# Optimization experiments

Hardware: AMD Instinct MI355X
Metric: run time of the kernel (lower is better)

## Reference

```python
import jax, jax.numpy as jnp
import numpy as np

B, L, IN, H, E = 64, 255, 32, 256, 128
PAD = (L - 1) // 2
DN = ('NCH', 'OIH', 'NCH')


def setup_inputs() -> dict:
    ks = jax.random.split(jax.random.key(0), 10)
    r = lambda k, shp, s=0.05: jax.random.normal(k, shp, dtype=jnp.float32) * s
    return {
        's': jax.random.normal(ks[0], (B, L, IN), dtype=jnp.float32),
        'conv1_w': r(ks[1], (H, IN, L)),
        'conv1_b': r(ks[2], (H,)),
        'bn_gamma': jnp.ones((H,), jnp.float32),
        'bn_beta': jnp.zeros((H,), jnp.float32),
        'conv2_w': r(ks[3], (E, H, L)),
        'conv2_b': r(ks[4], (E,)),
        'pw1': r(ks[5], (E, H, L)),   # stacked Linear(L, H) weights, one per channel
        'pb1': r(ks[6], (E, H)),
        'pw2': r(ks[7], (E, 2, H)),   # stacked Linear(H, 2) weights
        'pb2': r(ks[8], (E, 2)),
    }


def reference(s, conv1_w, conv1_b, bn_gamma, bn_beta, conv2_w, conv2_b, pw1, pb1, pw2, pb2):
    x = jnp.transpose(s, (0, 2, 1))  # (B, IN, T)
    h = jax.lax.conv_general_dilated(x, conv1_w, (1,), [(PAD, PAD)], dimension_numbers=DN)
    h = jax.nn.relu(h + conv1_b[None, :, None])
    # BatchNorm1d in training mode: biased batch stats over (N, T)
    mean = h.mean(axis=(0, 2), keepdims=True)
    var = ((h - mean) ** 2).mean(axis=(0, 2), keepdims=True)
    h = (h - mean) * jax.lax.rsqrt(var + 1e-5) * bn_gamma[None, :, None] + bn_beta[None, :, None]
    z = jax.lax.conv_general_dilated(h, conv2_w, (1,), [(PAD, PAD)], dimension_numbers=DN)
    z = jnp.transpose(z + conv2_b[None, :, None], (0, 2, 1))  # (B, T, E)

    rf = jnp.fft.rfft(z, axis=1)                 # (B, F, E), F = L//2 + 1 == E
    power = jnp.abs(rf)[:, :, 1:] ** 2           # faithful channel-axis slice -> (B, F, E-1)
    freq_bins = jnp.fft.rfftfreq(L)[1:]          # (F-1,) == (E-1,)
    frequency = jnp.sum(freq_bins * power, axis=1) / jnp.sum(power, axis=1)  # (B, E-1)
    amplitude = 2.0 * jnp.sqrt(jnp.sum(power, axis=1)) / L                    # (B, E-1)
    offset = rf.real[:, :, 0] / L                                              # (B, E)

    # batched per-channel 2-layer MLP (replaces Python loop over embedding_dim)
    hmid = jax.nn.relu(jnp.einsum('btc,cht->bch', z, pw1) + pb1[None])  # (B, E, H)
    ang = jnp.einsum('bch,coh->bco', hmid, pw2) + pb2[None]             # (B, E, 2)
    phase = jnp.arctan2(ang[:, :, 1], ang[:, :, 0])                     # (B, E)
    return (amplitude, phase, frequency, offset)
```

## Files before the change

### kernel.cpp

```cpp
#include <hip/hip_runtime.h>
#include <math.h>

#define TB   64
#define TT   255
#define TIN  32
#define NH   256
#define NE   128
#define NK   255
#define NPAD 127

#define NF    384
#define NBINS 193
#define NFC   386
#define HCH   64

typedef __attribute__((ext_vector_type(8))) short short8;
typedef __attribute__((ext_vector_type(4))) float float4v;

#define WSB_WP1  0u
#define WSB_Z    0u
#define WSB_W2S  8388608u
#define WSB_HSP  21037056u
#define WSB_ZSP  27361280u
#define WSB_BD   40009728u
#define WSB_BW   40404992u
#define WSB_BI   40800256u
#define WSB_H    41811968u
#define WSB_HMID 41811968u
#define WSB_BN   58589184u

#define O_AMP   0u
#define O_PHASE 8128u
#define O_FREQ  16320u
#define O_OFF   24448u

static __device__ __forceinline__ unsigned short f2bf(float f) {
  unsigned int u = __float_as_uint(f);
  unsigned int r = (u + 0x7FFFu + ((u >> 16) & 1u)) >> 16;
  return (unsigned short)r;
}
static __device__ __forceinline__ float bf2f(unsigned short s) {
  return __uint_as_float(((unsigned int)s) << 16);
}
static __device__ __forceinline__ short8 as_s8(uint4 v) {
  union { uint4 u; short8 s; } c; c.u = v; return c.s;
}

static __device__ __forceinline__ void stage8(unsigned int* __restrict__ U, int r,
                                              int p0, const float* __restrict__ v) {
  const int sw = r & 7;
  const int base = r * 32;
#pragma unroll
  for (int q = 0; q < 4; ++q) {
    float x0 = v[2 * q], x1 = v[2 * q + 1];
    unsigned short h0 = f2bf(x0), h1 = f2bf(x1);
    unsigned short l0 = f2bf(x0 - bf2f(h0)), l1 = f2bf(x1 - bf2f(h1));
    int p = p0 + q;
    U[base + ((((p >> 2) ^ sw) << 2) | (p & 3))] = (unsigned int)h0 | ((unsigned int)h1 << 16);
    U[base + (((((p >> 2) + 4) ^ sw) << 2) | (p & 3))] = (unsigned int)l0 | ((unsigned int)l1 << 16);
  }
}
static __device__ __forceinline__ short8 frag(const unsigned short* __restrict__ lds,
                                              int row, int quad, int part) {
  return *(const short8*)&lds[row * 64 + (((quad ^ (part << 2)) ^ (row & 7)) << 3)];
}
#define MF(a, b, c) __builtin_amdgcn_mfma_f32_16x16x32_bf16((a), (b), (c), 0, 0, 0)

__global__ __launch_bounds__(256) void bn_zero_k(float* __restrict__ bn) {
  bn[threadIdx.x] = 0.f;
  bn[256 + threadIdx.x] = 0.f;
}

__global__ __launch_bounds__(256) void basis_init_k(float* __restrict__ bd,
                                                    float* __restrict__ bw,
                                                    float* __restrict__ bi) {
  const int m = blockIdx.x;
  const int t = threadIdx.x;
  const int f = m >> 1, im = m & 1;
  const float C = 6.28318530717958647692f / 384.f;
  int r1 = (f * t) % 384;
  float th1 = C * (float)r1;
  float s1 = sinf(th1), c1 = cosf(th1);
  bd[m * 256 + t] = im ? -s1 : c1;
  float wgt = (f == 0 || f == 192) ? 1.f : 2.f;
  bi[m * 256 + t] = (im ? -s1 * wgt : c1 * wgt) * (1.f / 384.f);
  int a = f * (t - 127);
  int r2 = a % 384; if (r2 < 0) r2 += 384;
  float th2 = C * (float)r2;
  bw[m * 256 + t] = im ? sinf(th2) : cosf(th2);
}

__global__ __launch_bounds__(256) void pack1_k(const float* __restrict__ w1,
                                               unsigned int* __restrict__ wp1u) {
  __shared__ float tile[512][33];
  const int et = blockIdx.x, kc = blockIdx.y;
  const int kk0 = kc * 32, cnt = min(32, NK - kk0);
  const int tid = threadIdx.x;
  for (int idx = tid; idx < 512 * 32; idx += 256) {
    int row = idx >> 5, kl = idx & 31;
    if (kl < cnt) {
      int e_l = row >> 5, i_l = row & 31;
      tile[row][kl] = w1[(size_t)((et * 16 + e_l) * TIN + i_l) * NK + kk0 + kl];
    }
  }
  __syncthreads();
  const int lane = tid >> 2, jp = (tid & 3) * 2;
  const int row0 = (lane & 15) * 32 + (lane >> 4) * 8 + jp;
  for (int kl = 0; kl < cnt; ++kl) {
    float w0 = tile[row0][kl], w1v = tile[row0 + 1][kl];
    unsigned short h0 = f2bf(w0), h1 = f2bf(w1v);
    unsigned short l0 = f2bf(w0 - bf2f(h0)), l1 = f2bf(w1v - bf2f(h1));
    size_t base = (size_t)(kk0 + kl) * 8192 + et * 512 + tid;
    wp1u[base] = (unsigned int)h0 | ((unsigned int)h1 << 16);
    wp1u[base + 256] = (unsigned int)l0 | ((unsigned int)l1 << 16);
  }
}

#define C1_ROWS 384
__global__ __launch_bounds__(256, 2) void conv1_mfma(
    const float* __restrict__ s, const unsigned int* __restrict__ wp1u,
    const float* __restrict__ b1v, float* __restrict__ hf, float* __restrict__ bn) {
  __shared__ __align__(16) unsigned short Alds[C1_ROWS * 64];
  const int th = blockIdx.x & 1, chg = blockIdx.x >> 1, b = blockIdx.y;
  const int tid = threadIdx.x, lane = tid & 63, wv = tid >> 6;
  const int quad = lane >> 4, l15 = lane & 15;
  const int tg = wv & 1, eg = wv >> 1;
  unsigned int* Au = (unsigned int*)Alds;

  for (int idx = tid; idx < C1_ROWS * 16; idx += 256) {
    int r = idx >> 4, p = idx & 15;
    int t = th * 128 + r - NPAD;
    float v0 = 0.f, v1 = 0.f;
    if (t >= 0 && t < TT) {
      const float* sp = &s[(size_t)(b * TT + t) * TIN + p * 2];
      v0 = sp[0]; v1 = sp[1];
    }
    unsigned short h0 = f2bf(v0), h1 = f2bf(v1);
    unsigned short l0 = f2bf(v0 - bf2f(h0)), l1 = f2bf(v1 - bf2f(h1));
    int sw = r & 7;
    Au[r * 32 + ((((p >> 2) ^ sw) << 2) | (p & 3))] = (unsigned int)h0 | ((unsigned int)h1 << 16);
    Au[r * 32 + (((((p >> 2) + 4) ^ sw) << 2) | (p & 3))] = (unsigned int)l0 | ((unsigned int)l1 << 16);
  }

#define LOADB1(buf, KK) do {                                                      \
    const uint4* _b = (const uint4*)(wp1u + (size_t)(KK) * 8192u) +               \
                      (chg * 4 + eg * 2) * 128;                                   \
    buf[0] = _b[lane];          buf[1] = _b[64 + lane];                           \
    buf[2] = _b[128 + lane];    buf[3] = _b[192 + lane];                          \
  } while (0)

#define MSTEP1(KK, buf) do {                                                      \
    short8 bh0 = as_s8(buf[0]), bl0 = as_s8(buf[1]);                              \
    short8 bh1 = as_s8(buf[2]), bl1 = as_s8(buf[3]);                              \
    _Pragma("unroll")                                                             \
    for (int mi = 0; mi < 4; ++mi) {                                              \
      const int row = tg * 64 + mi * 16 + l15 + (KK);                             \
      const int sw = row & 7;                                                     \
      short8 ah = *(const short8*)&Alds[row * 64 + ((quad ^ sw) << 3)];           \
      short8 al = *(const short8*)&Alds[row * 64 + (((quad ^ 4) ^ sw) << 3)];     \
      acc[mi][0] = MF(ah, bh0, acc[mi][0]);                                       \
      acc[mi][0] = MF(ah, bl0, acc[mi][0]);                                       \
      acc[mi][0] = MF(al, bh0, acc[mi][0]);                                       \
      acc[mi][1] = MF(ah, bh1, acc[mi][1]);                                       \
      acc[mi][1] = MF(ah, bl1, acc[mi][1]);                                       \
      acc[mi][1] = MF(al, bh1, acc[mi][1]);                                       \
    }                                                                             \
  } while (0)

  uint4 b0[4], b1x[4], b2x[4];
  LOADB1(b0, 0);
  LOADB1(b1x, 1);
  LOADB1(b2x, 2);
  __syncthreads();

  float4v acc[4][2];
#pragma unroll
  for (int mi = 0; mi < 4; ++mi)
#pragma unroll
    for (int ni = 0; ni < 2; ++ni) acc[mi][ni] = (float4v)(0.f);

  for (int kp = 0; kp < 84; ++kp) {
    const int kk = kp * 3;
    MSTEP1(kk, b0);     LOADB1(b0, kk + 3);
    MSTEP1(kk + 1, b1x); LOADB1(b1x, kk + 4);
    MSTEP1(kk + 2, b2x); LOADB1(b2x, kk + 5);
  }
  MSTEP1(252, b0);
  MSTEP1(253, b1x);
  MSTEP1(254, b2x);

  float s1[2] = {0.f, 0.f}, s2[2] = {0.f, 0.f};
#pragma unroll
  for (int mi = 0; mi < 4; ++mi) {
#pragma unroll
    for (int ni = 0; ni < 2; ++ni) {
      int ch = chg * 64 + (eg * 2 + ni) * 16 + l15;
      float bias = b1v[ch];
#pragma unroll
      for (int r = 0; r < 4; ++r) {
        int t = th * 128 + tg * 64 + mi * 16 + quad * 4 + r;
        if (t < TT) {
          float v = fmaxf(acc[mi][ni][r] + bias, 0.f);
          hf[(size_t)(b * 256 + t) * NH + ch] = v;
          s1[ni] += v; s2[ni] += v * v;
        }
      }
    }
  }
#pragma unroll
  for (int ni = 0; ni < 2; ++ni) {
    s1[ni] += __shfl_xor(s1[ni], 16);
    s1[ni] += __shfl_xor(s1[ni], 32);
    s2[ni] += __shfl_xor(s2[ni], 16);
    s2[ni] += __shfl_xor(s2[ni], 32);
    if (quad == 0) {
      int ch = chg * 64 + (eg * 2 + ni) * 16 + l15;
      atomicAdd(&bn[ch], s1[ni]);
      atomicAdd(&bn[256 + ch], s2[ni]);
    }
  }
#undef LOADB1
#undef MSTEP1
}

__global__ __launch_bounds__(256) void bn_final_k(const float* __restrict__ gamma,
                                                  const float* __restrict__ beta,
                                                  float* __restrict__ bn) {
  const int h = threadIdx.x;
  const float inv = 1.0f / (TB * TT);
  float m = bn[h] * inv;
  float var = bn[256 + h] * inv - m * m;
  float sc = gamma[h] / sqrtf(var + 1e-5f);
  bn[512 + h] = sc;
  bn[768 + h] = beta[h] - m * sc;
}

__global__ __launch_bounds__(256, 2) void w2prep_mfma(
    const float* __restrict__ w2, const float* __restrict__ bw,
    float* __restrict__ outw, int h0c) {
  __shared__ __align__(16) unsigned short Alds[128 * 64];
  __shared__ __align__(16) unsigned short Blds[128 * 64];
  const int hc = blockIdx.x;
  const int m0 = blockIdx.y * 128;
  const int tid = threadIdx.x, lane = tid & 63, wv = tid >> 6;
  const int quad = lane >> 4, l15 = lane & 15;
  const int wm = wv >> 1, wn = wv & 1;
  unsigned int* Au = (unsigned int*)Alds;
  unsigned int* Bu = (unsigned int*)Blds;

  float4v acc[4][4];
#pragma unroll
  for (int i = 0; i < 4; ++i)
#pragma unroll
    for (int j = 0; j < 4; ++j) acc[i][j] = (float4v)(0.f);

  const int rA = tid >> 1, hfA = tid & 1;
  const int fcA = m0 + rA;
  const float* srcA = bw + fcA * 256;
  const int rB = tid >> 1, hfB = tid & 1;
  const float* srcB = w2 + ((size_t)(rB * NH + h0c + hc)) * NK;

  for (int kk = 0; kk < 8; ++kk) {
    const int k0 = kk * 32;
    if (kk) __syncthreads();
    {
      float va[16];
      if (fcA < NFC) {
        const float4* s4 = (const float4*)(srcA + k0 + hfA * 16);
        *(float4*)(va + 0) = s4[0]; *(float4*)(va + 4) = s4[1];
        *(float4*)(va + 8) = s4[2]; *(float4*)(va + 12) = s4[3];
      } else {
#pragma unroll
        for (int q = 0; q < 16; ++q) va[q] = 0.f;
      }
      stage8(Au, rA, hfA * 8, va);
      stage8(Au, rA, hfA * 8 + 4, va + 8);
    }
    {
      float vb[16];
#pragma unroll
      for (int q = 0; q < 16; ++q) {
        int k = k0 + hfB * 16 + q;
        vb[q] = (k < NK) ? srcB[k] : 0.f;
      }
      stage8(Bu, rB, hfB * 8, vb);
      stage8(Bu, rB, hfB * 8 + 4, vb + 8);
    }
    __syncthreads();
    short8 bh[4], bl[4];
#pragma unroll
    for (int ni = 0; ni < 4; ++ni) {
      int rb = wn * 64 + ni * 16 + l15;
      bh[ni] = frag(Blds, rb, quad, 0);
      bl[ni] = frag(Blds, rb, quad, 1);
    }
#pragma unroll
    for (int mi = 0; mi < 4; ++mi) {
      int ra = wm * 64 + mi * 16 + l15;
      short8 ah = frag(Alds, ra, quad, 0);
      short8 al = frag(Alds, ra, quad, 1);
#pragma unroll
      for (int ni = 0; ni < 4; ++ni) {
        acc[mi][ni] = MF(ah, bh[ni], acc[mi][ni]);
        acc[mi][ni] = MF(ah, bl[ni], acc[mi][ni]);
        acc[mi][ni] = MF(al, bh[ni], acc[mi][ni]);
      }
    }
  }
#pragma unroll
  for (int mi = 0; mi < 4; ++mi) {
    int fc0 = m0 + wm * 64 + mi * 16 + quad * 4;
#pragma unroll
    for (int ni = 0; ni < 4; ++ni) {
      int n = hc * 128 + wn * 64 + ni * 16 + l15;
#pragma unroll
      for (int r = 0; r < 4; ++r) {
        if (fc0 + r < NFC) outw[(size_t)(fc0 + r) * 8192 + n] = acc[mi][ni][r];
      }
    }
  }
}

__global__ __launch_bounds__(256) void dft_k(const float* __restrict__ hf,
                                             const float* __restrict__ bn,
                                             const float* __restrict__ bd,
                                             float* __restrict__ outh, int h0) {
  __shared__ __align__(16) float Al[32][68];
  __shared__ __align__(16) float Bl[32][68];
  const int tid = threadIdx.x;
  const int m0 = blockIdx.y * 64;
  const int n0 = blockIdx.x * 64;
  const int b = n0 >> 6;
  const int tm = tid & 15, tn = tid >> 4;
  const int klA = tid & 31, mlA = tid >> 5;
  const int nlB = tid & 63, klB4 = tid >> 6;
  const float scL = bn[512 + h0 + nlB];
  const float shL = bn[768 + h0 + nlB];
  float acc[4][4];
#pragma unroll
  for (int i = 0; i < 4; ++i)
#pragma unroll
    for (int j = 0; j < 4; ++j) acc[i][j] = 0.f;

  for (int k0 = 0; k0 < TT; k0 += 32) {
    __syncthreads();
#pragma unroll
    for (int r = 0; r < 8; ++r) {
      int ml = r * 8 + mlA;
      int fc = m0 + ml;
      Al[klA][ml] = (fc < NFC) ? bd[fc * 256 + k0 + klA] : 0.f;
    }
#pragma unroll
    for (int r = 0; r < 8; ++r) {
      int kl = r * 4 + klB4;
      int t = k0 + kl;
      Bl[kl][nlB] = (t < TT)
          ? fmaf(hf[((size_t)b * 256 + t) * NH + h0 + nlB], scL, shL) : 0.f;
    }
    __syncthreads();
#pragma unroll
    for (int kt = 0; kt < 32; ++kt) {
      float4v a4 = *(const float4v*)&Al[kt][tm * 4];
      float4v b4 = *(const float4v*)&Bl[kt][tn * 4];
#pragma unroll
      for (int i = 0; i < 4; ++i)
#pragma unroll
        for (int j = 0; j < 4; ++j) acc[i][j] = fmaf(a4[i], b4[j], acc[i][j]);
    }
  }
#pragma unroll
  for (int i = 0; i < 4; ++i) {
    int fc = m0 + tm * 4 + i;
    if (fc < NFC) {
      float4v v; v[0] = acc[i][0]; v[1] = acc[i][1]; v[2] = acc[i][2]; v[3] = acc[i][3];
      *(float4v*)&outh[(size_t)fc * 4096 + n0 + tn * 4] = v;
    }
  }
}

__global__ __launch_bounds__(256) void fgemm_k(const float* __restrict__ outh,
                                               const float* __restrict__ outw,
                                               float* __restrict__ zsp, int first) {
  __shared__ __align__(16) float Ar[32][68];
  __shared__ __align__(16) float Ai[32][68];
  __shared__ __align__(16) float Br[32][68];
  __shared__ __align__(16) float Bi[32][68];
  const int f = blockIdx.y;
  const int e0 = blockIdx.x * 64;
  const int tid = threadIdx.x;
  const int tb = tid & 15, te = tid >> 4;
  const int klA = tid & 31, blA8 = tid >> 5;
  const int nlB = tid & 63, klB4 = tid >> 6;
  const float* Hre = outh + (size_t)(2 * f) * 4096;
  const float* Him = Hre + 4096;
  const float* Wre = outw + (size_t)(2 * f) * 8192;
  const float* Wim = Wre + 8192;
  float accr[4][4], acci[4][4];
#pragma unroll
  for (int i = 0; i < 4; ++i)
#pragma unroll
    for (int j = 0; j < 4; ++j) { accr[i][j] = 0.f; acci[i][j] = 0.f; }

  for (int k0 = 0; k0 < HCH; k0 += 32) {
    __syncthreads();
#pragma unroll
    for (int r = 0; r < 8; ++r) {
      int bl = r * 8 + blA8;
      Ar[klA][bl] = Hre[bl * 64 + k0 + klA];
      Ai[klA][bl] = Him[bl * 64 + k0 + klA];
      int kl = r * 4 + klB4;
      Br[kl][nlB] = Wre[(k0 + kl) * 128 + e0 + nlB];
      Bi[kl][nlB] = Wim[(k0 + kl) * 128 + e0 + nlB];
    }
    __syncthreads();
#pragma unroll
    for (int kt = 0; kt < 32; ++kt) {
      float4v ar = *(const float4v*)&Ar[kt][tb * 4];
      float4v ai = *(const float4v*)&Ai[kt][tb * 4];
      float4v br = *(const float4v*)&Br[kt][te * 4];
      float4v bi = *(const float4v*)&Bi[kt][te * 4];
#pragma unroll
      for (int i = 0; i < 4; ++i)
#pragma unroll
        for (int j = 0; j < 4; ++j) {
          accr[i][j] = fmaf(ar[i], br[j], accr[i][j]);
          accr[i][j] = fmaf(-ai[i], bi[j], accr[i][j]);
          acci[i][j] = fmaf(ar[i], bi[j], acci[i][j]);
          acci[i][j] = fmaf(ai[i], br[j], acci[i][j]);
        }
    }
  }
  float* Zr = zsp + (size_t)(2 * f) * 8192;
  float* Zi = Zr + 8192;
#pragma unroll
  for (int i = 0; i < 4; ++i) {
    int b = tb * 4 + i;
    size_t off = (size_t)b * 128 + e0 + te * 4;
    float4v vr; vr[0] = accr[i][0]; vr[1] = accr[i][1]; vr[2] = accr[i][2]; vr[3] = accr[i][3];
    float4v vi; vi[0] = acci[i][0]; vi[1] = acci[i][1]; vi[2] = acci[i][2]; vi[3] = acci[i][3];
    if (first) {
      *(float4v*)&Zr[off] = vr;
      *(float4v*)&Zi[off] = vi;
    } else {
      float4v or_ = *(const float4v*)&Zr[off];
      float4v oi_ = *(const float4v*)&Zi[off];
      *(float4v*)&Zr[off] = or_ + vr;
      *(float4v*)&Zi[off] = oi_ + vi;
    }
  }
}

__global__ __launch_bounds__(256) void idft_k(const float* __restrict__ zsp,
                                              const float* __restrict__ bi,
                                              const float* __restrict__ b2,
                                              float* __restrict__ z) {
  __shared__ __align__(16) float Al[32][68];
  __shared__ __align__(16) float Bl[32][68];
  const int tid = threadIdx.x;
  const int m0 = blockIdx.x * 64;
  const int n0 = blockIdx.y * 64;
  const int tm = tid & 15, tn = tid >> 4;
  const int mlA = tid & 63, klA4 = tid >> 6;
  float acc[4][4];
#pragma unroll
  for (int i = 0; i < 4; ++i)
#pragma unroll
    for (int j = 0; j < 4; ++j) acc[i][j] = 0.f;

  for (int k0 = 0; k0 < NFC; k0 += 32) {
    __syncthreads();
#pragma unroll
    for (int r = 0; r < 8; ++r) {
      int kl = r * 4 + klA4;
      int fc = k0 + kl;
      Al[kl][mlA] = (fc < NFC) ? zsp[(size_t)fc * 8192 + m0 + mlA] : 0.f;
      Bl[kl][mlA] = (fc < NFC) ? bi[fc * 256 + n0 + mlA] : 0.f;
    }
    __syncthreads();
#pragma unroll
    for (int kt = 0; kt < 32; ++kt) {
      float4v a4 = *(const float4v*)&Al[kt][tm * 4];
      float4v b4 = *(const float4v*)&Bl[kt][tn * 4];
#pragma unroll
      for (int i = 0; i < 4; ++i)
#pragma unroll
        for (int j = 0; j < 4; ++j) acc[i][j] = fmaf(a4[i], b4[j], acc[i][j]);
    }
  }
#pragma unroll
  for (int i = 0; i < 4; ++i) {
    int be = m0 + tm * 4 + i;
    float bv = b2[be & 127];
#pragma unroll
    for (int j = 0; j < 4; ++j) {
      int t = n0 + tn * 4 + j;
      if (t < TT) z[(size_t)be * TT + t] = acc[i][j] + bv;
    }
  }
}

__global__ __launch_bounds__(256) void mlp1_k(const float* __restrict__ z,
                                              const float* __restrict__ pw1,
                                              const float* __restrict__ pb1,
                                              float* __restrict__ hmid) {
  const int TC = 128;
  __shared__ float zl[TC * 68];
  __shared__ float pl[TC * 68];
  const int c = blockIdx.y, h0 = blockIdx.x * 64, tid = threadIdx.x;
  const int h4 = tid & 15, b4 = tid >> 4;
  float acc[4][4];
#pragma unroll
  for (int a = 0; a < 4; ++a)
#pragma unroll
    for (int bb = 0; bb < 4; ++bb) acc[a][bb] = 0.f;
  for (int t0 = 0; t0 < TT; t0 += TC) {
    const int tc = min(TC, TT - t0);
    __syncthreads();
    for (int idx = tid; idx < 64 * tc; idx += 256) {
      int r = idx / tc, t = idx - r * tc;
      zl[t * 68 + r] = z[(size_t)(r * NE + c) * TT + t0 + t];
      pl[t * 68 + r] = pw1[(size_t)(c * NH + h0 + r) * TT + t0 + t];
    }
    __syncthreads();
    for (int t = 0; t < tc; ++t) {
      float4 zv = *(const float4*)&zl[t * 68 + b4 * 4];
      float4 pv = *(const float4*)&pl[t * 68 + h4 * 4];
      float zz[4] = {zv.x, zv.y, zv.z, zv.w};
      float pp[4] = {pv.x, pv.y, pv.z, pv.w};
#pragma unroll
      for (int a = 0; a < 4; ++a)
#pragma unroll
        for (int bb = 0; bb < 4; ++bb) acc[a][bb] = fmaf(pp[a], zz[bb], acc[a][bb]);
    }
  }
#pragma unroll
  for (int a = 0; a < 4; ++a) {
    int hh = h0 + h4 * 4 + a;
    float bias = pb1[c * NH + hh];
#pragma unroll
    for (int bb = 0; bb < 4; ++bb) {
      int bidx = b4 * 4 + bb;
      float v = acc[a][bb] + bias;
      hmid[(size_t)(bidx * NE + c) * NH + hh] = fmaxf(v, 0.f);
    }
  }
}

__global__ __launch_bounds__(256) void mlp2_k(const float* __restrict__ hmid,
                                              const float* __restrict__ pw2,
                                              const float* __restrict__ pb2,
                                              float* __restrict__ out) {
  const int tid = threadIdx.x, lane = tid & 63, wv = tid >> 6;
  const int p = blockIdx.x * 4 + wv;
  const int b = p >> 7, c = p & 127;
  const float4 hv = *(const float4*)&hmid[(size_t)(b * NE + c) * NH + lane * 4];
  const float4 p0 = *(const float4*)&pw2[(size_t)(c * 2 + 0) * NH + lane * 4];
  const float4 p1 = *(const float4*)&pw2[(size_t)(c * 2 + 1) * NH + lane * 4];
  float s0 = hv.x * p0.x + hv.y * p0.y + hv.z * p0.z + hv.w * p0.w;
  float s1 = hv.x * p1.x + hv.y * p1.y + hv.z * p1.z + hv.w * p1.w;
#pragma unroll
  for (int off = 32; off; off >>= 1) {
    s0 += __shfl_down(s0, off);
    s1 += __shfl_down(s1, off);
  }
  if (lane == 0) {
    float a0 = s0 + pb2[c * 2 + 0];
    float a1 = s1 + pb2[c * 2 + 1];
    out[O_PHASE + b * NE + c] = atan2f(a1, a0);
  }
}

__global__ __launch_bounds__(256) void amp_k(const float* __restrict__ z,
                                             float* __restrict__ out) {
  const int tid = threadIdx.x, lane = tid & 63, wv = tid >> 6;
  const int b = blockIdx.x, c = blockIdx.y * 4 + wv;
  const float* row = z + (size_t)(b * NE + c) * TT;
  float s1 = 0.f, s2 = 0.f;
  for (int idx = lane; idx < TT; idx += 64) {
    float v = row[idx];
    s1 += v; s2 += v * v;
  }
#pragma unroll
  for (int off = 32; off; off >>= 1) {
    s1 += __shfl_down(s1, off);
    s2 += __shfl_down(s2, off);
  }
  if (lane == 0 && c >= 1) {
    float P = 0.5f * (255.f * s2 + s1 * s1);
    out[O_AMP + b * 127 + (c - 1)] = 2.f * sqrtf(P) / 255.f;
    out[O_FREQ + b * 127 + (c - 1)] = (float)c / 255.f;
  }
}

__global__ __launch_bounds__(128) void offset_k(const float* __restrict__ z,
                                                float* __restrict__ out) {
  __shared__ float zr[TT];
  __shared__ float ct[TT];
  const int b = blockIdx.x, tid = threadIdx.x;
  for (int idx = tid; idx < TT; idx += 128) {
    zr[idx] = z[(size_t)(b * NE + 0) * TT + idx];
    ct[idx] = cosf(6.283185307179586f * (float)idx / 255.f);
  }
  __syncthreads();
  const int f = tid;
  float s = 0.f;
  int m = 0;
  for (int t = 0; t < TT; ++t) {
    s += zr[t] * ct[m];
    m += f; if (m >= TT) m -= TT;
  }
  out[O_OFF + b * NE + f] = s / 255.f;
}

extern "C" void kernel_launch(void* const* d_in, const int* in_sizes, int n_in,
                              void* d_out, int out_size, void* d_ws, size_t ws_size,
                              hipStream_t stream) {
  (void)in_sizes; (void)n_in; (void)out_size; (void)ws_size;
  const float* s       = (const float*)d_in[0];
  const float* conv1_w = (const float*)d_in[1];
  const float* conv1_b = (const float*)d_in[2];
  const float* bn_g    = (const float*)d_in[3];
  const float* bn_b    = (const float*)d_in[4];
  const float* conv2_w = (const float*)d_in[5];
  const float* conv2_b = (const float*)d_in[6];
  const float* pw1     = (const float*)d_in[7];
  const float* pb1     = (const float*)d_in[8];
  const float* pw2     = (const float*)d_in[9];
  const float* pb2     = (const float*)d_in[10];
  float* out = (float*)d_out;
  char* ws   = (char*)d_ws;

  unsigned int* wp1u = (unsigned int*)(ws + WSB_WP1);
  float* hf   = (float*)(ws + WSB_H);
  float* z    = (float*)(ws + WSB_Z);
  float* bn   = (float*)(ws + WSB_BN);
  float* hmid = (float*)(ws + WSB_HMID);
  float* w2s  = (float*)(ws + WSB_W2S);
  float* hsp  = (float*)(ws + WSB_HSP);
  float* zsp  = (float*)(ws + WSB_ZSP);
  float* bd   = (float*)(ws + WSB_BD);
  float* bwt  = (float*)(ws + WSB_BW);
  float* bit  = (float*)(ws + WSB_BI);

  bn_zero_k<<<1, 256, 0, stream>>>(bn);
  basis_init_k<<<NFC, 256, 0, stream>>>(bd, bwt, bit);
  pack1_k<<<dim3(16, 8), 256, 0, stream>>>(conv1_w, wp1u);

  conv1_mfma<<<dim3(8, TB), 256, 0, stream>>>(s, wp1u, conv1_b, hf, bn);
  bn_final_k<<<1, 256, 0, stream>>>(bn_g, bn_b, bn);

  for (int c = 0; c < 4; ++c) {
    w2prep_mfma<<<dim3(64, 4), 256, 0, stream>>>(conv2_w, bwt, w2s, c * HCH);
    dft_k<<<dim3(64, 7), 256, 0, stream>>>(hf, bn, bd, hsp, c * HCH);
    fgemm_k<<<dim3(2, NBINS), 256, 0, stream>>>(hsp, w2s, zsp, c == 0 ? 1 : 0);
  }
  idft_k<<<dim3(128, 4), 256, 0, stream>>>(zsp, bit, conv2_b, z);

  mlp1_k<<<dim3(4, NE), 256, 0, stream>>>(z, pw1, pb1, hmid);
  mlp2_k<<<TB * NE / 4, 256, 0, stream>>>(hmid, pw2, pb2, out);
  amp_k<<<dim3(TB, 32), 256, 0, stream>>>(z, out);
  offset_k<<<TB, 128, 0, stream>>>(z, out);
}
```

Baseline: 668.0 us.

## Port DFT, frequency GEMM and inverse DFT to split-bf16 MFMA kernels

Replaces the scalar fp32 FMA GEMMs used for the forward DFT of the BN output, the complex per-frequency GEMM and the inverse DFT with MFMA kernels. Each operand is split into three bf16 parts, giving six MFMAs per tile. The w2prep kernel also moves from the two-part split (three MFMAs) to this three-part split. Workspace layout changes, the inverse basis is stored transposed and padded, and basis entries at t=255 are zeroed. The aim is to use the matrix cores for FLOP-heavy stages that were limited by vector ALU, at the cost of more MFMA work, LDS, and extra split conversion during staging.

```diff
diff --git a/kernel.cpp b/kernel.cpp
--- a/kernel.cpp
+++ b/kernel.cpp
@@ -12,6 +12,7 @@
 #define NF    384
 #define NBINS 193
 #define NFC   386
+#define FCP   416
 #define HCH   64
 
 typedef __attribute__((ext_vector_type(8))) short short8;
@@ -19,15 +20,15 @@
 
 #define WSB_WP1  0u
 #define WSB_Z    0u
-#define WSB_W2S  8388608u
-#define WSB_HSP  21037056u
-#define WSB_ZSP  27361280u
-#define WSB_BD   40009728u
-#define WSB_BW   40404992u
-#define WSB_BI   40800256u
-#define WSB_H    41811968u
-#define WSB_HMID 41811968u
-#define WSB_BN   58589184u
+#define WSB_HF   8388608u
+#define WSB_HMID 8388608u
+#define WSB_W2S  25165824u
+#define WSB_HSP  37814272u
+#define WSB_ZSP  44138496u
+#define WSB_BD   56786944u
+#define WSB_BW   57182208u
+#define WSB_BIT  57577472u
+#define WSB_BN   58003456u
 
 #define O_AMP   0u
 #define O_PHASE 8128u
@@ -44,6 +45,14 @@
 }
 static __device__ __forceinline__ short8 as_s8(uint4 v) {
   union { uint4 u; short8 s; } c; c.u = v; return c.s;
+}
+
+static __device__ __forceinline__ void split3(float x, unsigned short& h,
+                                              unsigned short& l, unsigned short& m2) {
+  h = f2bf(x);
+  float r1 = x - bf2f(h);
+  l = f2bf(r1);
+  m2 = f2bf(r1 - bf2f(l));
 }
 
 static __device__ __forceinline__ void stage8(unsigned int* __restrict__ U, int r,
@@ -60,11 +69,51 @@
     U[base + (((((p >> 2) + 4) ^ sw) << 2) | (p & 3))] = (unsigned int)l0 | ((unsigned int)l1 << 16);
   }
 }
+
+static __device__ __forceinline__ void stage8_3(unsigned int* __restrict__ U,
+                                                unsigned int* __restrict__ U2, int r,
+                                                int p0, const float* __restrict__ v) {
+  const int sw = r & 7;
+  const int base = r * 32;
+#pragma unroll
+  for (int q = 0; q < 4; ++q) {
+    unsigned short h0, l0, m0_, h1, l1, m1_;
+    split3(v[2 * q], h0, l0, m0_);
+    split3(v[2 * q + 1], h1, l1, m1_);
+    int p = p0 + q;
+    int shi = (((p >> 2) ^ sw) << 2) | (p & 3);
+    int slo = ((((p >> 2) + 4) ^ sw) << 2) | (p & 3);
+    U[base + shi] = (unsigned int)h0 | ((unsigned int)h1 << 16);
+    U[base + slo] = (unsigned int)l0 | ((unsigned int)l1 << 16);
+    U2[base + shi] = (unsigned int)m0_ | ((unsigned int)m1_ << 16);
+  }
+}
+static __device__ __forceinline__ void stage2_3(unsigned int* __restrict__ U,
+                                                unsigned int* __restrict__ U2, int r,
+                                                int p, float x0, float x1) {
+  const int sw = r & 7;
+  unsigned short h0, l0, m0_, h1, l1, m1_;
+  split3(x0, h0, l0, m0_);
+  split3(x1, h1, l1, m1_);
+  int shi = (((p >> 2) ^ sw) << 2) | (p & 3);
+  int slo = ((((p >> 2) + 4) ^ sw) << 2) | (p & 3);
+  U[r * 32 + shi] = (unsigned int)h0 | ((unsigned int)h1 << 16);
+  U[r * 32 + slo] = (unsigned int)l0 | ((unsigned int)l1 << 16);
+  U2[r * 32 + shi] = (unsigned int)m0_ | ((unsigned int)m1_ << 16);
+}
 static __device__ __forceinline__ short8 frag(const unsigned short* __restrict__ lds,
                                               int row, int quad, int part) {
   return *(const short8*)&lds[row * 64 + (((quad ^ (part << 2)) ^ (row & 7)) << 3)];
 }
 #define MF(a, b, c) __builtin_amdgcn_mfma_f32_16x16x32_bf16((a), (b), (c), 0, 0, 0)
+#define MF6(accv, ahv, alv, a2v, bhv, blv, b2v) do {                              \
+    accv = MF(ahv, bhv, accv);                                                    \
+    accv = MF(ahv, blv, accv);                                                    \
+    accv = MF(alv, bhv, accv);                                                    \
+    accv = MF(alv, blv, accv);                                                    \
+    accv = MF(ahv, b2v, accv);                                                    \
+    accv = MF(a2v, bhv, accv);                                                    \
+  } while (0)
 
 __global__ __launch_bounds__(256) void bn_zero_k(float* __restrict__ bn) {
   bn[threadIdx.x] = 0.f;
@@ -73,7 +122,7 @@
 
 __global__ __launch_bounds__(256) void basis_init_k(float* __restrict__ bd,
                                                     float* __restrict__ bw,
-                                                    float* __restrict__ bi) {
+                                                    float* __restrict__ bi_t) {
   const int m = blockIdx.x;
   const int t = threadIdx.x;
   const int f = m >> 1, im = m & 1;
@@ -81,13 +130,16 @@
   int r1 = (f * t) % 384;
   float th1 = C * (float)r1;
   float s1 = sinf(th1), c1 = cosf(th1);
-  bd[m * 256 + t] = im ? -s1 : c1;
+  float vd = im ? -s1 : c1;
+  bd[m * 256 + t] = (t == 255) ? 0.f : vd;
   float wgt = (f == 0 || f == 192) ? 1.f : 2.f;
-  bi[m * 256 + t] = (im ? -s1 * wgt : c1 * wgt) * (1.f / 384.f);
+  bi_t[t * FCP + m] = (im ? -s1 * wgt : c1 * wgt) * (1.f / 384.f);
+  if (m < FCP - NFC) bi_t[t * FCP + NFC + m] = 0.f;
   int a = f * (t - 127);
   int r2 = a % 384; if (r2 < 0) r2 += 384;
   float th2 = C * (float)r2;
-  bw[m * 256 + t] = im ? sinf(th2) : cosf(th2);
+  float vw = im ? sinf(th2) : cosf(th2);
+  bw[m * 256 + t] = (t == 255) ? 0.f : vw;
 }
 
 __global__ __launch_bounds__(256) void pack1_k(const float* __restrict__ w1,
@@ -235,18 +287,22 @@
   bn[768 + h] = beta[h] - m * sc;
 }
 
+
 __global__ __launch_bounds__(256, 2) void w2prep_mfma(
     const float* __restrict__ w2, const float* __restrict__ bw,
-    float* __restrict__ outw, int h0c) {
+    float* __restrict__ W, int h0c) {
   __shared__ __align__(16) unsigned short Alds[128 * 64];
+  __shared__ __align__(16) unsigned short A2lds[128 * 64];
   __shared__ __align__(16) unsigned short Blds[128 * 64];
-  const int hc = blockIdx.x;
-  const int m0 = blockIdx.y * 128;
+  __shared__ __align__(16) unsigned short B2lds[128 * 64];
+  const int n0 = blockIdx.x * 128, m0 = blockIdx.y * 128;
   const int tid = threadIdx.x, lane = tid & 63, wv = tid >> 6;
   const int quad = lane >> 4, l15 = lane & 15;
   const int wm = wv >> 1, wn = wv & 1;
   unsigned int* Au = (unsigned int*)Alds;
+  unsigned int* A2u = (unsigned int*)A2lds;
   unsigned int* Bu = (unsigned int*)Blds;
+  unsigned int* B2u = (unsigned int*)B2lds;
 
   float4v acc[4][4];
 #pragma unroll
@@ -258,7 +314,8 @@
   const int fcA = m0 + rA;
   const float* srcA = bw + fcA * 256;
   const int rB = tid >> 1, hfB = tid & 1;
-  const float* srcB = w2 + ((size_t)(rB * NH + h0c + hc)) * NK;
+  const int eB = (n0 + rB) >> 6, hlB = (n0 + rB) & 63;
+  const float* srcB = w2 + ((size_t)(eB * NH + h0c + hlB)) * NK;
 
   for (int kk = 0; kk < 8; ++kk) {
     const int k0 = kk * 32;
@@ -273,8 +330,8 @@
 #pragma unroll
         for (int q = 0; q < 16; ++q) va[q] = 0.f;
       }
-      stage8(Au, rA, hfA * 8, va);
-      stage8(Au, rA, hfA * 8 + 4, va + 8);
+      stage8_3(Au, A2u, rA, hfA * 8, va);
+      stage8_3(Au, A2u, rA, hfA * 8 + 4, va + 8);
     }
     {
       float vb[16];
@@ -283,28 +340,26 @@
         int k = k0 + hfB * 16 + q;
         vb[q] = (k < NK) ? srcB[k] : 0.f;
       }
-      stage8(Bu, rB, hfB * 8, vb);
-      stage8(Bu, rB, hfB * 8 + 4, vb + 8);
+      stage8_3(Bu, B2u, rB, hfB * 8, vb);
+      stage8_3(Bu, B2u, rB, hfB * 8 + 4, vb + 8);
     }
     __syncthreads();
-    short8 bh[4], bl[4];
+    short8 bh[4], bl[4], b2[4];
 #pragma unroll
     for (int ni = 0; ni < 4; ++ni) {
       int rb = wn * 64 + ni * 16 + l15;
       bh[ni] = frag(Blds, rb, quad, 0);
       bl[ni] = frag(Blds, rb, quad, 1);
+      b2[ni] = frag(B2lds, rb, quad, 0);
     }
 #pragma unroll
     for (int mi = 0; mi < 4; ++mi) {
       int ra = wm * 64 + mi * 16 + l15;
       short8 ah = frag(Alds, ra, quad, 0);
       short8 al = frag(Alds, ra, quad, 1);
-#pragma unroll
-      for (int ni = 0; ni < 4; ++ni) {
-        acc[mi][ni] = MF(ah, bh[ni], acc[mi][ni]);
-        acc[mi][ni] = MF(ah, bl[ni], acc[mi][ni]);
-        acc[mi][ni] = MF(al, bh[ni], acc[mi][ni]);
-      }
+      short8 a2 = frag(A2lds, ra, quad, 0);
+#pragma unroll
+      for (int ni = 0; ni < 4; ++ni) MF6(acc[mi][ni], ah, al, a2, bh[ni], bl[ni], b2[ni]);
     }
   }
 #pragma unroll
@@ -312,189 +367,266 @@
     int fc0 = m0 + wm * 64 + mi * 16 + quad * 4;
 #pragma unroll
     for (int ni = 0; ni < 4; ++ni) {
-      int n = hc * 128 + wn * 64 + ni * 16 + l15;
+      int n = n0 + wn * 64 + ni * 16 + l15;
 #pragma unroll
       for (int r = 0; r < 4; ++r) {
-        if (fc0 + r < NFC) outw[(size_t)(fc0 + r) * 8192 + n] = acc[mi][ni][r];
-      }
-    }
-  }
-}
-
-__global__ __launch_bounds__(256) void dft_k(const float* __restrict__ hf,
-                                             const float* __restrict__ bn,
-                                             const float* __restrict__ bd,
-                                             float* __restrict__ outh, int h0) {
-  __shared__ __align__(16) float Al[32][68];
-  __shared__ __align__(16) float Bl[32][68];
-  const int tid = threadIdx.x;
-  const int m0 = blockIdx.y * 64;
-  const int n0 = blockIdx.x * 64;
-  const int b = n0 >> 6;
-  const int tm = tid & 15, tn = tid >> 4;
-  const int klA = tid & 31, mlA = tid >> 5;
-  const int nlB = tid & 63, klB4 = tid >> 6;
-  const float scL = bn[512 + h0 + nlB];
-  const float shL = bn[768 + h0 + nlB];
-  float acc[4][4];
+        if (fc0 + r < NFC) W[(size_t)(fc0 + r) * 8192 + n] = acc[mi][ni][r];
+      }
+    }
+  }
+}
+
+__global__ __launch_bounds__(256, 2) void dftH_mfma(
+    const float* __restrict__ hf, const float* __restrict__ bn,
+    const float* __restrict__ bd, float* __restrict__ H, int h0c) {
+  __shared__ __align__(16) unsigned short Alds[128 * 64];
+  __shared__ __align__(16) unsigned short A2lds[128 * 64];
+  __shared__ __align__(16) unsigned short Blds[128 * 64];
+  __shared__ __align__(16) unsigned short B2lds[128 * 64];
+  const int n0 = blockIdx.x * 128, m0 = blockIdx.y * 128;
+  const int b0 = n0 >> 6;
+  const int tid = threadIdx.x, lane = tid & 63, wv = tid >> 6;
+  const int quad = lane >> 4, l15 = lane & 15;
+  const int wm = wv >> 1, wn = wv & 1;
+  const int g = tid >> 6;
+  unsigned int* Au = (unsigned int*)Alds;
+  unsigned int* A2u = (unsigned int*)A2lds;
+  unsigned int* Bu = (unsigned int*)Blds;
+  unsigned int* B2u = (unsigned int*)B2lds;
+  const float scL = bn[512 + h0c + lane];
+  const float shL = bn[768 + h0c + lane];
+
+  float4v acc[4][4];
 #pragma unroll
   for (int i = 0; i < 4; ++i)
 #pragma unroll
-    for (int j = 0; j < 4; ++j) acc[i][j] = 0.f;
-
-  for (int k0 = 0; k0 < TT; k0 += 32) {
+    for (int j = 0; j < 4; ++j) acc[i][j] = (float4v)(0.f);
+
+  const int rA = tid >> 1, hfA = tid & 1;
+  const int fcA = m0 + rA;
+  const float* srcA = bd + fcA * 256;
+
+  for (int kk = 0; kk < 8; ++kk) {
+    const int k0 = kk * 32;
+    if (kk) __syncthreads();
+    {
+      float va[16];
+      if (fcA < NFC) {
+        const float4* s4 = (const float4*)(srcA + k0 + hfA * 16);
+        *(float4*)(va + 0) = s4[0]; *(float4*)(va + 4) = s4[1];
+        *(float4*)(va + 8) = s4[2]; *(float4*)(va + 12) = s4[3];
+      } else {
+#pragma unroll
+        for (int q = 0; q < 16; ++q) va[q] = 0.f;
+      }
+      stage8_3(Au, A2u, rA, hfA * 8, va);
+      stage8_3(Au, A2u, rA, hfA * 8 + 4, va + 8);
+    }
+#pragma unroll
+    for (int i = 0; i < 8; ++i) {
+      int combo = i * 4 + g;
+      int tp = combo >> 1, bl_ = combo & 1;
+      int t0 = k0 + tp * 2;
+      int b = b0 + bl_;
+      float v0 = (t0 < TT)
+          ? fmaf(hf[(size_t)(b * 256 + t0) * NH + h0c + lane], scL, shL) : 0.f;
+      float v1 = (t0 + 1 < TT)
+          ? fmaf(hf[(size_t)(b * 256 + t0 + 1) * NH + h0c + lane], scL, shL) : 0.f;
+      stage2_3(Bu, B2u, bl_ * 64 + lane, tp, v0, v1);
+    }
     __syncthreads();
-#pragma unroll
-    for (int r = 0; r < 8; ++r) {
-      int ml = r * 8 + mlA;
-      int fc = m0 + ml;
-      Al[klA][ml] = (fc < NFC) ? bd[fc * 256 + k0 + klA] : 0.f;
-    }
-#pragma unroll
-    for (int r = 0; r < 8; ++r) {
-      int kl = r * 4 + klB4;
-      int t = k0 + kl;
-      Bl[kl][nlB] = (t < TT)
-          ? fmaf(hf[((size_t)b * 256 + t) * NH + h0 + nlB], scL, shL) : 0.f;
+    short8 bh[4], bl[4], b2[4];
+#pragma unroll
+    for (int ni = 0; ni < 4; ++ni) {
+      int rb = wn * 64 + ni * 16 + l15;
+      bh[ni] = frag(Blds, rb, quad, 0);
+      bl[ni] = frag(Blds, rb, quad, 1);
+      b2[ni] = frag(B2lds, rb, quad, 0);
+    }
+#pragma unroll
+    for (int mi = 0; mi < 4; ++mi) {
+      int ra = wm * 64 + mi * 16 + l15;
+      short8 ah = frag(Alds, ra, quad, 0);
+      short8 al = frag(Alds, ra, quad, 1);
+      short8 a2 = frag(A2lds, ra, quad, 0);
+#pragma unroll
+      for (int ni = 0; ni < 4; ++ni) MF6(acc[mi][ni], ah, al, a2, bh[ni], bl[ni], b2[ni]);
+    }
+  }
+#pragma unroll
+  for (int mi = 0; mi < 4; ++mi) {
+    int fc0 = m0 + wm * 64 + mi * 16 + quad * 4;
+#pragma unroll
+    for (int ni = 0; ni < 4; ++ni) {
+      int n = n0 + wn * 64 + ni * 16 + l15;
+#pragma unroll
+      for (int r = 0; r < 4; ++r) {
+        if (fc0 + r < NFC) H[(size_t)(fc0 + r) * 4096 + n] = acc[mi][ni][r];
+      }
+    }
+  }
+}
+
+__global__ __launch_bounds__(256, 2) void fgemm_mfma(
+    const float* __restrict__ H, const float* __restrict__ W,
+    float* __restrict__ zsp, int first) {
+  __shared__ __align__(16) unsigned short Alds[64 * 64];
+  __shared__ __align__(16) unsigned short A2lds[64 * 64];
+  __shared__ __align__(16) unsigned short Blds[128 * 64];
+  __shared__ __align__(16) unsigned short B2lds[128 * 64];
+  const int ri = blockIdx.x, f = blockIdx.y;
+  const int tid = threadIdx.x, lane = tid & 63, wv = tid >> 6;
+  const int quad = lane >> 4, l15 = lane & 15;
+  const int wm = wv >> 1, wn = wv & 1;
+  unsigned int* Au = (unsigned int*)Alds;
+  unsigned int* A2u = (unsigned int*)A2lds;
+  unsigned int* Bu = (unsigned int*)Blds;
+  unsigned int* B2u = (unsigned int*)B2lds;
+
+  float4v acc[2][4];
+#pragma unroll
+  for (int i = 0; i < 2; ++i)
+#pragma unroll
+    for (int j = 0; j < 4; ++j) acc[i][j] = (float4v)(0.f);
+
+  const int rA = tid >> 2, qA = tid & 3;
+  const int rB = tid >> 1, hB = tid & 1;
+
+  for (int kk = 0; kk < 4; ++kk) {
+    const int ca = kk >> 1;
+    const int hb = (kk & 1) * 32;
+    if (kk) __syncthreads();
+    {
+      float va[8];
+      const float4* s4 = (const float4*)(H + (size_t)(2 * f + ca) * 4096 + rA * 64 + hb + qA * 8);
+      *(float4*)(va + 0) = s4[0]; *(float4*)(va + 4) = s4[1];
+      stage8_3(Au, A2u, rA, qA * 4, va);
+    }
+    {
+      const int cb = ri ^ (kk >> 1);
+      const int neg = (ri == 0 && kk >= 2);
+      float vb[16];
+      const float4* s4 = (const float4*)(W + (size_t)(2 * f + cb) * 8192 + rB * 64 + hb + hB * 16);
+      *(float4*)(vb + 0) = s4[0]; *(float4*)(vb + 4) = s4[1];
+      *(float4*)(vb + 8) = s4[2]; *(float4*)(vb + 12) = s4[3];
+      if (neg) {
+#pragma unroll
+        for (int q = 0; q < 16; ++q) vb[q] = -vb[q];
+      }
+      stage8_3(Bu, B2u, rB, hB * 8, vb);
+      stage8_3(Bu, B2u, rB, hB * 8 + 4, vb + 8);
     }
     __syncthreads();
-#pragma unroll
-    for (int kt = 0; kt < 32; ++kt) {
-      float4v a4 = *(const float4v*)&Al[kt][tm * 4];
-      float4v b4 = *(const float4v*)&Bl[kt][tn * 4];
-#pragma unroll
-      for (int i = 0; i < 4; ++i)
-#pragma unroll
-        for (int j = 0; j < 4; ++j) acc[i][j] = fmaf(a4[i], b4[j], acc[i][j]);
-    }
-  }
-#pragma unroll
-  for (int i = 0; i < 4; ++i) {
-    int fc = m0 + tm * 4 + i;
-    if (fc < NFC) {
-      float4v v; v[0] = acc[i][0]; v[1] = acc[i][1]; v[2] = acc[i][2]; v[3] = acc[i][3];
-      *(float4v*)&outh[(size_t)fc * 4096 + n0 + tn * 4] = v;
-    }
-  }
-}
-
-__global__ __launch_bounds__(256) void fgemm_k(const float* __restrict__ outh,
-                                               const float* __restrict__ outw,
-                                               float* __restrict__ zsp, int first) {
-  __shared__ __align__(16) float Ar[32][68];
-  __shared__ __align__(16) float Ai[32][68];
-  __shared__ __align__(16) float Br[32][68];
-  __shared__ __align__(16) float Bi[32][68];
-  const int f = blockIdx.y;
-  const int e0 = blockIdx.x * 64;
-  const int tid = threadIdx.x;
-  const int tb = tid & 15, te = tid >> 4;
-  const int klA = tid & 31, blA8 = tid >> 5;
-  const int nlB = tid & 63, klB4 = tid >> 6;
-  const float* Hre = outh + (size_t)(2 * f) * 4096;
-  const float* Him = Hre + 4096;
-  const float* Wre = outw + (size_t)(2 * f) * 8192;
-  const float* Wim = Wre + 8192;
-  float accr[4][4], acci[4][4];
+    short8 bh[4], bl[4], b2[4];
+#pragma unroll
+    for (int ni = 0; ni < 4; ++ni) {
+      int rb = wn * 64 + ni * 16 + l15;
+      bh[ni] = frag(Blds, rb, quad, 0);
+      bl[ni] = frag(Blds, rb, quad, 1);
+      b2[ni] = frag(B2lds, rb, quad, 0);
+    }
+#pragma unroll
+    for (int mi = 0; mi < 2; ++mi) {
+      int ra = wm * 32 + mi * 16 + l15;
+      short8 ah = frag(Alds, ra, quad, 0);
+      short8 al = frag(Alds, ra, quad, 1);
+      short8 a2 = frag(A2lds, ra, quad, 0);
+#pragma unroll
+      for (int ni = 0; ni < 4; ++ni) MF6(acc[mi][ni], ah, al, a2, bh[ni], bl[ni], b2[ni]);
+    }
+  }
+  float* Z = zsp + (size_t)(2 * f + ri) * 8192;
+#pragma unroll
+  for (int mi = 0; mi < 2; ++mi) {
+#pragma unroll
+    for (int ni = 0; ni < 4; ++ni) {
+      int e = wn * 64 + ni * 16 + l15;
+#pragma unroll
+      for (int r = 0; r < 4; ++r) {
+        int b = wm * 32 + mi * 16 + quad * 4 + r;
+        size_t off = (size_t)b * 128 + e;
+        if (first) Z[off] = acc[mi][ni][r];
+        else       Z[off] += acc[mi][ni][r];
+      }
+    }
+  }
+}
+
+__global__ __launch_bounds__(256, 2) void idft_mfma(
+    const float* __restrict__ zsp, const float* __restrict__ bi_t,
+    const float* __restrict__ b2, float* __restrict__ z) {
+  __shared__ __align__(16) unsigned short Alds[128 * 64];
+  __shared__ __align__(16) unsigned short A2lds[128 * 64];
+  __shared__ __align__(16) unsigned short Blds[128 * 64];
+  __shared__ __align__(16) unsigned short B2lds[128 * 64];
+  const int n0 = blockIdx.x * 128, m0 = blockIdx.y * 128;
+  const int tid = threadIdx.x, lane = tid & 63, wv = tid >> 6;
+  const int quad = lane >> 4, l15 = lane & 15;
+  const int wm = wv >> 1, wn = wv & 1;
+  const int g = tid >> 6;
+  unsigned int* Au = (unsigned int*)Alds;
+  unsigned int* A2u = (unsigned int*)A2lds;
+  unsigned int* Bu = (unsigned int*)Blds;
+  unsigned int* B2u = (unsigned int*)B2lds;
+
+  float4v acc[4][4];
 #pragma unroll
   for (int i = 0; i < 4; ++i)
 #pragma unroll
-    for (int j = 0; j < 4; ++j) { accr[i][j] = 0.f; acci[i][j] = 0.f; }
-
-  for (int k0 = 0; k0 < HCH; k0 += 32) {
+    for (int j = 0; j < 4; ++j) acc[i][j] = (float4v)(0.f);
+
+  const int rB = tid >> 1, hB = tid & 1;
+
+  for (int kk = 0; kk < 13; ++kk) {
+    const int k0 = kk * 32;
+    if (kk) __syncthreads();
+#pragma unroll
+    for (int i = 0; i < 8; ++i) {
+      int combo = i * 4 + g;
+      int tp = combo >> 1, beh = combo & 1;
+      int fc0 = k0 + tp * 2;
+      int row = beh * 64 + lane;
+      float v0 = (fc0 < NFC) ? zsp[(size_t)fc0 * 8192 + m0 + row] : 0.f;
+      float v1 = (fc0 + 1 < NFC) ? zsp[(size_t)(fc0 + 1) * 8192 + m0 + row] : 0.f;
+      stage2_3(Au, A2u, row, tp, v0, v1);
+    }
+    {
+      float vb[16];
+      const float4* s4 = (const float4*)(bi_t + (size_t)(n0 + rB) * FCP + k0 + hB * 16);
+      *(float4*)(vb + 0) = s4[0]; *(float4*)(vb + 4) = s4[1];
+      *(float4*)(vb + 8) = s4[2]; *(float4*)(vb + 12) = s4[3];
+      stage8_3(Bu, B2u, rB, hB * 8, vb);
+      stage8_3(Bu, B2u, rB, hB * 8 + 4, vb + 8);
+    }
     __syncthreads();
-#pragma unroll
-    for (int r = 0; r < 8; ++r) {
-      int bl = r * 8 + blA8;
-      Ar[klA][bl] = Hre[bl * 64 + k0 + klA];
-      Ai[klA][bl] = Him[bl * 64 + k0 + klA];
-      int kl = r * 4 + klB4;
-      Br[kl][nlB] = Wre[(k0 + kl) * 128 + e0 + nlB];
-      Bi[kl][nlB] = Wim[(k0 + kl) * 128 + e0 + nlB];
-    }
-    __syncthreads();
-#pragma unroll
-    for (int kt = 0; kt < 32; ++kt) {
-      float4v ar = *(const float4v*)&Ar[kt][tb * 4];
-      float4v ai = *(const float4v*)&Ai[kt][tb * 4];
-      float4v br = *(const float4v*)&Br[kt][te * 4];
-      float4v bi = *(const float4v*)&Bi[kt][te * 4];
-#pragma unroll
-      for (int i = 0; i < 4; ++i)
-#pragma unroll
-        for (int j = 0; j < 4; ++j) {
-          accr[i][j] = fmaf(ar[i], br[j], accr[i][j]);
-          accr[i][j] = fmaf(-ai[i], bi[j], accr[i][j]);
-          acci[i][j] = fmaf(ar[i], bi[j], acci[i][j]);
-          acci[i][j] = fmaf(ai[i], br[j], acci[i][j]);
-        }
-    }
-  }
-  float* Zr = zsp + (size_t)(2 * f) * 8192;
-  float* Zi = Zr + 8192;
-#pragma unroll
-  for (int i = 0; i < 4; ++i) {
-    int b = tb * 4 + i;
-    size_t off = (size_t)b * 128 + e0 + te * 4;
-    float4v vr; vr[0] = accr[i][0]; vr[1] = accr[i][1]; vr[2] = accr[i][2]; vr[3] = accr[i][3];
-    float4v vi; vi[0] = acci[i][0]; vi[1] = acci[i][1]; vi[2] = acci[i][2]; vi[3] = acci[i][3];
-    if (first) {
-      *(float4v*)&Zr[off] = vr;
-      *(float4v*)&Zi[off] = vi;
-    } else {
-      float4v or_ = *(const float4v*)&Zr[off];
-      float4v oi_ = *(const float4v*)&Zi[off];
-      *(float4v*)&Zr[off] = or_ + vr;
-      *(float4v*)&Zi[off] = oi_ + vi;
-    }
-  }
-}
-
-__global__ __launch_bounds__(256) void idft_k(const float* __restrict__ zsp,
-                                              const float* __restrict__ bi,
-                                              const float* __restrict__ b2,
-                                              float* __restrict__ z) {
-  __shared__ __align__(16) float Al[32][68];
-  __shared__ __align__(16) float Bl[32][68];
-  const int tid = threadIdx.x;
-  const int m0 = blockIdx.x * 64;
-  const int n0 = blockIdx.y * 64;
-  const int tm = tid & 15, tn = tid >> 4;
-  const int mlA = tid & 63, klA4 = tid >> 6;
-  float acc[4][4];
-#pragma unroll
-  for (int i = 0; i < 4; ++i)
-#pragma unroll
-    for (int j = 0; j < 4; ++j) acc[i][j] = 0.f;
-
-  for (int k0 = 0; k0 < NFC; k0 += 32) {
-    __syncthreads();
-#pragma unroll
-    for (int r = 0; r < 8; ++r) {
-      int kl = r * 4 + klA4;
-      int fc = k0 + kl;
-      Al[kl][mlA] = (fc < NFC) ? zsp[(size_t)fc * 8192 + m0 + mlA] : 0.f;
-      Bl[kl][mlA] = (fc < NFC) ? bi[fc * 256 + n0 + mlA] : 0.f;
-    }
-    __syncthreads();
-#pragma unroll
-    for (int kt = 0; kt < 32; ++kt) {
-      float4v a4 = *(const float4v*)&Al[kt][tm * 4];
-      float4v b4 = *(const float4v*)&Bl[kt][tn * 4];
-#pragma unroll
-      for (int i = 0; i < 4; ++i)
-#pragma unroll
-        for (int j = 0; j < 4; ++j) acc[i][j] = fmaf(a4[i], b4[j], acc[i][j]);
-    }
-  }
-#pragma unroll
-  for (int i = 0; i < 4; ++i) {
-    int be = m0 + tm * 4 + i;
-    float bv = b2[be & 127];
-#pragma unroll
-    for (int j = 0; j < 4; ++j) {
-      int t = n0 + tn * 4 + j;
-      if (t < TT) z[(size_t)be * TT + t] = acc[i][j] + bv;
+    short8 bh[4], bl[4], b2[4];
+#pragma unroll
+    for (int ni = 0; ni < 4; ++ni) {
+      int rb = wn * 64 + ni * 16 + l15;
+      bh[ni] = frag(Blds, rb, quad, 0);
+      bl[ni] = frag(Blds, rb, quad, 1);
+      b2[ni] = frag(B2lds, rb, quad, 0);
+    }
+#pragma unroll
+    for (int mi = 0; mi < 4; ++mi) {
+      int ra = wm * 64 + mi * 16 + l15;
+      short8 ah = frag(Alds, ra, quad, 0);
+      short8 al = frag(Alds, ra, quad, 1);
+      short8 a2 = frag(A2lds, ra, quad, 0);
+#pragma unroll
+      for (int ni = 0; ni < 4; ++ni) MF6(acc[mi][ni], ah, al, a2, bh[ni], bl[ni], b2[ni]);
+    }
+  }
+#pragma unroll
+  for (int mi = 0; mi < 4; ++mi) {
+#pragma unroll
+    for (int ni = 0; ni < 4; ++ni) {
+      int t = n0 + wn * 64 + ni * 16 + l15;
+#pragma unroll
+      for (int r = 0; r < 4; ++r) {
+        int be = m0 + wm * 64 + mi * 16 + quad * 4 + r;
+        if (t < TT) z[(size_t)be * TT + t] = acc[mi][ni][r] + b2[be & 127];
+      }
     }
   }
 }
@@ -631,16 +763,16 @@
   char* ws   = (char*)d_ws;
 
   unsigned int* wp1u = (unsigned int*)(ws + WSB_WP1);
-  float* hf   = (float*)(ws + WSB_H);
   float* z    = (float*)(ws + WSB_Z);
-  float* bn   = (float*)(ws + WSB_BN);
+  float* hf   = (float*)(ws + WSB_HF);
   float* hmid = (float*)(ws + WSB_HMID);
-  float* w2s  = (float*)(ws + WSB_W2S);
-  float* hsp  = (float*)(ws + WSB_HSP);
+  float* W2s  = (float*)(ws + WSB_W2S);
+  float* Hs   = (float*)(ws + WSB_HSP);
   float* zsp  = (float*)(ws + WSB_ZSP);
   float* bd   = (float*)(ws + WSB_BD);
   float* bwt  = (float*)(ws + WSB_BW);
-  float* bit  = (float*)(ws + WSB_BI);
+  float* bit  = (float*)(ws + WSB_BIT);
+  float* bn   = (float*)(ws + WSB_BN);
 
   bn_zero_k<<<1, 256, 0, stream>>>(bn);
   basis_init_k<<<NFC, 256, 0, stream>>>(bd, bwt, bit);
@@ -650,11 +782,11 @@
   bn_final_k<<<1, 256, 0, stream>>>(bn_g, bn_b, bn);
 
   for (int c = 0; c < 4; ++c) {
-    w2prep_mfma<<<dim3(64, 4), 256, 0, stream>>>(conv2_w, bwt, w2s, c * HCH);
-    dft_k<<<dim3(64, 7), 256, 0, stream>>>(hf, bn, bd, hsp, c * HCH);
-    fgemm_k<<<dim3(2, NBINS), 256, 0, stream>>>(hsp, w2s, zsp, c == 0 ? 1 : 0);
-  }
-  idft_k<<<dim3(128, 4), 256, 0, stream>>>(zsp, bit, conv2_b, z);
+    w2prep_mfma<<<dim3(64, 4), 256, 0, stream>>>(conv2_w, bwt, W2s, c * HCH);
+    dftH_mfma<<<dim3(32, 4), 256, 0, stream>>>(hf, bn, bd, Hs, c * HCH);
+    fgemm_mfma<<<dim3(2, NBINS), 256, 0, stream>>>(Hs, W2s, zsp, c == 0 ? 1 : 0);
+  }
+  idft_mfma<<<dim3(2, 64), 256, 0, stream>>>(zsp, bit, conv2_b, z);
 
   mlp1_k<<<dim3(4, NE), 256, 0, stream>>>(z, pw1, pb1, hmid);
   mlp2_k<<<TB * NE / 4, 256, 0, stream>>>(hmid, pw2, pb2, out);
```

New measurement: 725.8 us. 1.09x slower.
